# Kernel tuning notes

Hardware: AMD Instinct MI355X
Metric: run time of the kernel (lower is better)

## Reference

```python
import jax, jax.numpy as jnp
import numpy as np

B, T, C, H = 2, 2048, 1024, 16  # head_dim for V = C//H = 64; QK head dim = 3


def setup_inputs() -> dict:
    key = jax.random.key(0)
    ks = jax.random.split(key, 6)
    x = jax.random.normal(ks[0], (B, T, C), dtype=jnp.float32)
    wq = jax.random.normal(ks[1], (C, H * 3), dtype=jnp.float32) * (C ** -0.5)
    wk = jax.random.normal(ks[2], (C, H * 3), dtype=jnp.float32) * (C ** -0.5)
    wv = jax.random.normal(ks[3], (C, C), dtype=jnp.float32) * (C ** -0.5)
    wo = jax.random.normal(ks[4], (C, C), dtype=jnp.float32) * (C ** -0.5)
    dirs = jax.random.normal(ks[5], (H, 3), dtype=jnp.float32)
    head_dirs = dirs / jnp.linalg.norm(dirs, axis=1, keepdims=True)  # unit trigram dirs
    scale = jnp.full((1,), 1.0 / np.sqrt(3.0), dtype=jnp.float32)
    return {"x": x, "wq": wq, "wk": wk, "wv": wv, "wo": wo,
            "head_dirs": head_dirs, "scale": scale}


def reference(x, wq, wk, wv, wo, head_dirs, scale):
    b, t, c = x.shape
    h = head_dirs.shape[0]
    hd = c // h
    # projections: QK live in a 3-dim geometric space per head
    q3 = (x @ wq).reshape(b, t, h, 3).transpose(0, 2, 1, 3)   # (B,H,T,3)
    k3 = (x @ wk).reshape(b, t, h, 3).transpose(0, 2, 1, 3)   # (B,H,T,3)
    v = (x @ wv).reshape(b, t, h, hd).transpose(0, 2, 1, 3)   # (B,H,T,hd)
    # projections of q,k onto per-head trigram directions
    q_on_dir = jnp.einsum('bhtd,hd->bht', q3, head_dirs)      # (B,H,T)
    k_on_dir = jnp.einsum('bhtd,hd->bht', k3, head_dirs)      # (B,H,T)
    dot_scores = jnp.einsum('bhtd,bhsd->bhts', q3, k3) * scale  # (B,H,T,T)
    geo_bias = q_on_dir[..., :, None] * k_on_dir[..., None, :]  # outer product bias
    scores = dot_scores + geo_bias
    causal = jnp.tril(jnp.ones((t, t), dtype=bool))
    scores = jnp.where(causal, scores, -jnp.inf)
    attn = jax.nn.softmax(scores, axis=-1)  # dropout p=0 -> identity
    out = jnp.einsum('bhts,bhsd->bhtd', attn, v)
    out = out.transpose(0, 2, 1, 3).reshape(b, t, c)
    return out @ wo
```

## Files before the change

kernel.cpp:

```cpp
#include <hip/hip_runtime.h>
#include <hip/hip_bf16.h>


typedef short bf16x8 __attribute__((ext_vector_type(8)));
typedef float f32x4 __attribute__((ext_vector_type(4)));
typedef __hip_bfloat16 bf16_t;
typedef unsigned int __attribute__((address_space(1))) u32_as1;
typedef unsigned int __attribute__((address_space(3))) u32_as3;

#define T_SEQ 2048
#define NHEAD 16
#define CDIM 1024
#define L2E 1.4426950408889634f

__device__ __forceinline__ void gl_lds16(const void* g, void* l) {
  __builtin_amdgcn_global_load_lds((const u32_as1*)g, (u32_as3*)l, 16, 0, 0);
}

__device__ __forceinline__ f32x4 mfma16(bf16x8 a, bf16x8 b, f32x4 c) {
  return __builtin_amdgcn_mfma_f32_16x16x32_bf16(a, b, c, 0, 0, 0);
}

__device__ __forceinline__ unsigned short f2bf(float f) {
  __hip_bfloat16 h = __float2bfloat16(f);
  return *(unsigned short*)&h;
}

__device__ __forceinline__ float fast_exp2(float x) {
#if __has_builtin(__builtin_amdgcn_exp2f)
  return __builtin_amdgcn_exp2f(x);
#else
  return exp2f(x);
#endif
}

__global__ __launch_bounds__(256) void k_prep(const float* __restrict__ x,
                                              const float* __restrict__ wq,
                                              const float* __restrict__ wk,
                                              const float* __restrict__ wv,
                                              const float* __restrict__ wo,
                                              bf16_t* __restrict__ xb,
                                              bf16_t* __restrict__ wqkT,
                                              bf16_t* __restrict__ wvT,
                                              bf16_t* __restrict__ woT) {
  __shared__ bf16_t tile[32][33];
  int bid = blockIdx.x, tid = threadIdx.x;
  if (bid < 4096) {
    int i = bid * 256 + tid;
    float4 v = ((const float4*)x)[i];
    ushort4 o;
    o.x = f2bf(v.x); o.y = f2bf(v.y); o.z = f2bf(v.z); o.w = f2bf(v.w);
    ((ushort4*)xb)[i] = o;
    return;
  }
  const float* src; bf16_t* dst; int R, C, bx, by;
  if (bid < 5120)      { int t = bid - 4096; src = wv; dst = wvT;            R = 1024; C = 1024; bx = t & 31; by = t >> 5; }
  else if (bid < 6144) { int t = bid - 5120; src = wo; dst = woT;            R = 1024; C = 1024; bx = t & 31; by = t >> 5; }
  else if (bid < 6208) { int t = bid - 6144; src = wq; dst = wqkT;           R = 1024; C = 48;   bx = t & 1;  by = t >> 1; }
  else                 { int t = bid - 6208; src = wk; dst = wqkT + 48*1024; R = 1024; C = 48;   bx = t & 1;  by = t >> 1; }
  int tx = tid & 31, ty = tid >> 5;
  int r0 = by * 32, c0 = bx * 32;
#pragma unroll
  for (int j = 0; j < 32; j += 8) {
    int r = r0 + ty + j, c = c0 + tx;
    if (r < R && c < C) tile[ty + j][tx] = __float2bfloat16(src[(size_t)r * C + c]);
  }
  __syncthreads();
#pragma unroll
  for (int j = 0; j < 32; j += 8) {
    int c = c0 + ty + j, r = r0 + tx;
    if (r < R && c < C) dst[(size_t)c * R + r] = tile[tx][ty + j];
  }
}

__global__ __launch_bounds__(256) void k_qkproj(const bf16_t* __restrict__ xb,
                                                const bf16_t* __restrict__ wqkT,
                                                const float* __restrict__ head_dirs,
                                                const float* __restrict__ scale,
                                                float* __restrict__ Qt,
                                                float* __restrict__ Kt) {
  __shared__ float red[4][16][96];
  int tid = threadIdx.x, wave = tid >> 6, lane = tid & 63;
  int g = lane >> 4, li = lane & 15;
  int m0 = blockIdx.x * 16;
  f32x4 acc[6] = {};
  int kb = wave * 256;
  for (int k0 = kb; k0 < kb + 256; k0 += 32) {
    bf16x8 a = *(const bf16x8*)(xb + (size_t)(m0 + li) * 1024 + k0 + g * 8);
#pragma unroll
    for (int nt = 0; nt < 6; ++nt) {
      bf16x8 bb = *(const bf16x8*)(wqkT + (size_t)(nt * 16 + li) * 1024 + k0 + g * 8);
      acc[nt] = mfma16(a, bb, acc[nt]);
    }
  }
#pragma unroll
  for (int nt = 0; nt < 6; ++nt)
#pragma unroll
    for (int r = 0; r < 4; ++r) red[wave][g * 4 + r][nt * 16 + li] = acc[nt][r];
  __syncthreads();
  for (int i = tid; i < 16 * 96; i += 256) {
    int row = i / 96, col = i - (i / 96) * 96;
    float v = red[0][row][col] + red[1][row][col] + red[2][row][col] + red[3][row][col];
    if (col >= 48) {
      int n = col - 48;
      int h = n / 3, c = n - h * 3;
      int mg = m0 + row;
      int bb = mg >> 11, tt = mg & 2047;
      Kt[(((size_t)bb * NHEAD + h) * 3 + c) * T_SEQ + tt] = v;
    } else {
      red[0][row][col] = v;
    }
  }
  __syncthreads();
  int row = tid >> 4, h = tid & 15;
  float q0 = red[0][row][h * 3 + 0];
  float q1 = red[0][row][h * 3 + 1];
  float q2 = red[0][row][h * 3 + 2];
  float d0 = head_dirs[h * 3 + 0];
  float d1 = head_dirs[h * 3 + 1];
  float d2 = head_dirs[h * 3 + 2];
  float sc = scale[0] * L2E;
  float dot = (q0 * d0 + q1 * d1 + q2 * d2) * L2E;
  int mg = m0 + row;
  int bb = mg >> 11, tt = mg & 2047;
  size_t base = ((size_t)bb * NHEAD + h) * 3 * T_SEQ + tt;
  Qt[base] = sc * q0 + d0 * dot;
  Qt[base + T_SEQ] = sc * q1 + d1 * dot;
  Qt[base + 2 * T_SEQ] = sc * q2 + d2 * dot;
}

__global__ __launch_bounds__(256) void k_gemm_bt(const bf16_t* __restrict__ A,
                                                 const bf16_t* __restrict__ Bt,
                                                 void* __restrict__ Cout,
                                                 int M, int N, int K, int mode) {
  __shared__ alignas(16) bf16_t As[2][64 * 32];
  __shared__ alignas(16) bf16_t Bs[2][128 * 32];
  int tid = threadIdx.x, wave = tid >> 6, lane = tid & 63;
  int g = lane >> 4, li = lane & 15;
  int n0 = blockIdx.x * 128, m0 = blockIdx.y * 64;
  int wm = wave >> 1, wn = wave & 1;

  const bf16_t* gA0 = A + (size_t)(m0 + (tid >> 2)) * K + (tid & 3) * 8;
  const bf16_t* gB0 = Bt + (size_t)(n0 + (tid >> 2)) * K + (tid & 3) * 8;
  const bf16_t* gB1 = Bt + (size_t)(n0 + 64 + (tid >> 2)) * K + (tid & 3) * 8;

#define GSTAGE(bufi, kk)                                                        \
  {                                                                             \
    gl_lds16(gA0 + (kk), (char*)&As[bufi][0] + (size_t)(wave * 64) * 16);       \
    gl_lds16(gB0 + (kk), (char*)&Bs[bufi][0] + (size_t)(wave * 64) * 16);       \
    gl_lds16(gB1 + (kk), (char*)&Bs[bufi][0] + (size_t)(256 + wave * 64) * 16); \
  }

  f32x4 acc[2][4] = {};
  GSTAGE(0, 0);

  for (int k0 = 0; k0 < K; k0 += 32) {
    int cur = (k0 >> 5) & 1;
    __syncthreads();
    if (k0 + 32 < K) GSTAGE(cur ^ 1, k0 + 32);
    bf16x8 af[2], bfr[4];
#pragma unroll
    for (int mt = 0; mt < 2; ++mt)
      af[mt] = *(const bf16x8*)&As[cur][(wm * 32 + mt * 16 + li) * 32 + g * 8];
#pragma unroll
    for (int nt = 0; nt < 4; ++nt)
      bfr[nt] = *(const bf16x8*)&Bs[cur][(wn * 64 + nt * 16 + li) * 32 + g * 8];
#pragma unroll
    for (int mt = 0; mt < 2; ++mt)
#pragma unroll
      for (int nt = 0; nt < 4; ++nt)
        acc[mt][nt] = mfma16(af[mt], bfr[nt], acc[mt][nt]);
  }
#undef GSTAGE

#pragma unroll
  for (int mt = 0; mt < 2; ++mt)
#pragma unroll
    for (int nt = 0; nt < 4; ++nt)
#pragma unroll
      for (int r = 0; r < 4; ++r) {
        int m = m0 + wm * 32 + mt * 16 + g * 4 + r;
        int n = n0 + wn * 64 + nt * 16 + li;
        float v = acc[mt][nt][r];
        if (mode == 0) {
          int bb = n >> 11, tt = n & 2047;
          ((bf16_t*)Cout)[((size_t)bb * 1024 + m) * T_SEQ + tt] = __float2bfloat16(v);
        } else {
          ((float*)Cout)[(size_t)m * N + n] = v;
        }
      }
}

__global__ __launch_bounds__(256, 4) void k_attn(const float* __restrict__ Qt,
                                                 const float* __restrict__ Kt,
                                                 const bf16_t* __restrict__ VT,
                                                 bf16_t* __restrict__ att) {
  __shared__ alignas(16) bf16_t Vb[2][2][64 * 64];
  __shared__ alignas(16) float Ks[2][3 * 128];
  int tid = threadIdx.x, wave = tid >> 6, lane = tid & 63;
  int g = lane >> 4, li = lane & 15;
  int bid = blockIdx.x;
  int qt = 31 - (bid >> 5);
  int bh = bid & 31;
  int b = bh >> 4, h = bh & 15;
  int mw = wave * 16;

  const float* Qp = Qt + (size_t)bh * 3 * T_SEQ;
  const float* Kp = Kt + (size_t)bh * 3 * T_SEQ;
  const bf16_t* Vp = VT + (size_t)bh * 64 * T_SEQ;

  int tq = qt * 64 + mw + li;
  float q0 = Qp[tq], q1 = Qp[T_SEQ + tq], q2 = Qp[2 * T_SEQ + tq];

  bf16x8 bones;
  unsigned short ob = (li == 0) ? (unsigned short)0x3F80 : (unsigned short)0;
#pragma unroll
  for (int j = 0; j < 8; ++j) bones[j] = (short)ob;

  const bf16_t* vg[2];
#pragma unroll
  for (int p = 0; p < 2; ++p) {
    int P = p * 256 + wave * 64 + lane;
    int d = P >> 3, c = (P & 7) ^ (d & 7);
    vg[p] = Vp + (size_t)d * T_SEQ + c * 8;
  }
  int kch = (wave == 3) ? lane : 32 + lane;
  const float* kg = Kp + (size_t)(kch >> 5) * T_SEQ + (kch & 31) * 4;
  int kbase = (wave == 3) ? 0 : 512;

#define STAGE(bufi, s0v)                                                      \
  {                                                                           \
    _Pragma("unroll") for (int sub_ = 0; sub_ < 2; ++sub_)                    \
        _Pragma("unroll") for (int p_ = 0; p_ < 2; ++p_)                      \
            gl_lds16(vg[p_] + (s0v) + sub_ * 64,                              \
                     (char*)&Vb[bufi][sub_][0] + (p_ * 256 + wave * 64) * 16);\
    if (wave >= 2) gl_lds16(kg + (s0v), (char*)&Ks[bufi][0] + kbase);         \
  }

#define BUILD_AFRAG(MASKED)                                                   \
  _Pragma("unroll") for (int half = 0; half < 2; ++half) {                    \
    int kb = sub * 64 + half * 32 + g * 8;                                    \
    f32x4 kv[3][2];                                                           \
    _Pragma("unroll") for (int c = 0; c < 3; ++c) {                           \
      kv[c][0] = *(const f32x4*)(ks + c * 128 + kb);                          \
      kv[c][1] = *(const f32x4*)(ks + c * 128 + kb + 4);                      \
    }                                                                         \
    _Pragma("unroll") for (int j = 0; j < 8; ++j) {                           \
      float scv = q0 * kv[0][j >> 2][j & 3] + q1 * kv[1][j >> 2][j & 3] +     \
                  q2 * kv[2][j >> 2][j & 3];                                  \
      float pv = fast_exp2(fminf(scv, 115.4f));                               \
      if (MASKED && (bkg + half * 32 + g * 8 + j > tq)) pv = 0.0f;            \
      afrag[half][j] = (short)f2bf(pv);                                       \
    }                                                                         \
  }

  int NT = (qt + 2) >> 1;
  STAGE(0, 0);

  f32x4 acc[5] = {};
  int sw = li & 7;
  int qmin = qt * 64 + mw;
  int qmax = qmin + 15;

  for (int st = 0; st < NT; ++st) {
    int buf = st & 1;
    __syncthreads();
    if (st + 1 < NT) STAGE(buf ^ 1, (st + 1) * 128);
    const float* ks = &Ks[buf][0];
#pragma unroll
    for (int sub = 0; sub < 2; ++sub) {
      int bkg = st * 128 + sub * 64;
      if (bkg > qmax) continue;
      bf16x8 afrag[2];
      if (bkg + 63 > qmin) { BUILD_AFRAG(1) } else { BUILD_AFRAG(0) }
      const bf16_t* vb = &Vb[buf][sub][0];
#pragma unroll
      for (int nt = 0; nt < 4; ++nt) {
        int row = nt * 16 + li;
        bf16x8 b0 = *(const bf16x8*)&vb[row * 64 + (g ^ sw) * 8];
        bf16x8 b1 = *(const bf16x8*)&vb[row * 64 + ((4 + g) ^ sw) * 8];
        acc[nt] = mfma16(afrag[0], b0, acc[nt]);
        acc[nt] = mfma16(afrag[1], b1, acc[nt]);
      }
      acc[4] = mfma16(afrag[0], bones, acc[4]);
      acc[4] = mfma16(afrag[1], bones, acc[4]);
    }
  }
#undef STAGE
#undef BUILD_AFRAG

  float linv[4];
#pragma unroll
  for (int r = 0; r < 4; ++r)
    linv[r] = 1.0f / fmaxf(__shfl(acc[4][r], lane & 48), 1e-35f);

#pragma unroll
  for (int nt = 0; nt < 4; ++nt)
#pragma unroll
    for (int r = 0; r < 4; ++r) {
      int t = qt * 64 + mw + g * 4 + r;
      att[((size_t)b * T_SEQ + t) * CDIM + h * 64 + nt * 16 + li] =
          __float2bfloat16(acc[nt][r] * linv[r]);
    }
}

extern "C" void kernel_launch(void* const* d_in, const int* in_sizes, int n_in,
                              void* d_out, int out_size, void* d_ws, size_t ws_size,
                              hipStream_t stream) {
  const float* x  = (const float*)d_in[0];
  const float* wq = (const float*)d_in[1];
  const float* wk = (const float*)d_in[2];
  const float* wv = (const float*)d_in[3];
  const float* wo = (const float*)d_in[4];
  const float* hd = (const float*)d_in[5];
  const float* sc = (const float*)d_in[6];
  float* out = (float*)d_out;

  char* ws = (char*)d_ws;
  bf16_t* wqkT = (bf16_t*)(ws + 0);
  bf16_t* wvT  = (bf16_t*)(ws + 196608);
  bf16_t* woT  = (bf16_t*)(ws + 2293760);
  float*  Qt   = (float*)(ws + 4390912);
  float*  Kt   = (float*)(ws + 5177344);
  bf16_t* VT   = (bf16_t*)(ws + 5963776);
  bf16_t* att  = (bf16_t*)(ws + 14352384);
  bf16_t* xb   = (bf16_t*)(ws + 22740992);

  k_prep<<<6272, 256, 0, stream>>>(x, wq, wk, wv, wo, xb, wqkT, wvT, woT);

  k_qkproj<<<256, 256, 0, stream>>>(xb, wqkT, hd, sc, Qt, Kt);

  k_gemm_bt<<<dim3(32, 16), 256, 0, stream>>>(wvT, xb, VT, 1024, 4096, 1024, 0);

  k_attn<<<1024, 256, 0, stream>>>(Qt, Kt, VT, att);

  k_gemm_bt<<<dim3(8, 64), 256, 0, stream>>>(att, woT, out, 4096, 1024, 1024, 1);
}
```

Measured before the change: 161.2 us.

## Double GEMM K-step to 64 and interleave causal attention tile order

The GEMM kernel now stages 64 K-elements per iteration instead of 32, so there are half as many barriers and more MFMAs per sync, at the cost of twice the shared memory per block. The attention kernel changes its block-to-query-tile mapping from strictly longest-first to an interleaved pattern that pairs short and long causal tiles. The goal is to balance work across CUs as blocks are dispatched, but it gives up the plain longest-first ordering, which may hurt tail balance.

```diff
diff --git a/kernel.cpp b/kernel.cpp
--- a/kernel.cpp
+++ b/kernel.cpp
@@ -133,8 +133,8 @@
                                                  const bf16_t* __restrict__ Bt,
                                                  void* __restrict__ Cout,
                                                  int M, int N, int K, int mode) {
-  __shared__ alignas(16) bf16_t As[2][64 * 32];
-  __shared__ alignas(16) bf16_t Bs[2][128 * 32];
+  __shared__ alignas(16) bf16_t As[2][2 * 64 * 32];
+  __shared__ alignas(16) bf16_t Bs[2][2 * 128 * 32];
   int tid = threadIdx.x, wave = tid >> 6, lane = tid & 63;
   int g = lane >> 4, li = lane & 15;
   int n0 = blockIdx.x * 128, m0 = blockIdx.y * 64;
@@ -144,32 +144,40 @@
   const bf16_t* gB0 = Bt + (size_t)(n0 + (tid >> 2)) * K + (tid & 3) * 8;
   const bf16_t* gB1 = Bt + (size_t)(n0 + 64 + (tid >> 2)) * K + (tid & 3) * 8;
 
-#define GSTAGE(bufi, kk)                                                        \
-  {                                                                             \
-    gl_lds16(gA0 + (kk), (char*)&As[bufi][0] + (size_t)(wave * 64) * 16);       \
-    gl_lds16(gB0 + (kk), (char*)&Bs[bufi][0] + (size_t)(wave * 64) * 16);       \
-    gl_lds16(gB1 + (kk), (char*)&Bs[bufi][0] + (size_t)(256 + wave * 64) * 16); \
+#define GSTAGE(bufi, kk)                                          \
+  {                                                               \
+    char* aB = (char*)&As[bufi][0];                               \
+    char* bB = (char*)&Bs[bufi][0];                               \
+    gl_lds16(gA0 + (kk), aB + tid * 16);                          \
+    gl_lds16(gA0 + (kk) + 32, aB + (256 + tid) * 16);             \
+    gl_lds16(gB0 + (kk), bB + tid * 16);                          \
+    gl_lds16(gB1 + (kk), bB + (256 + tid) * 16);                  \
+    gl_lds16(gB0 + (kk) + 32, bB + (512 + tid) * 16);             \
+    gl_lds16(gB1 + (kk) + 32, bB + (768 + tid) * 16);             \
   }
 
   f32x4 acc[2][4] = {};
   GSTAGE(0, 0);
 
-  for (int k0 = 0; k0 < K; k0 += 32) {
-    int cur = (k0 >> 5) & 1;
+  for (int k0 = 0; k0 < K; k0 += 64) {
+    int cur = (k0 >> 6) & 1;
     __syncthreads();
-    if (k0 + 32 < K) GSTAGE(cur ^ 1, k0 + 32);
-    bf16x8 af[2], bfr[4];
-#pragma unroll
-    for (int mt = 0; mt < 2; ++mt)
-      af[mt] = *(const bf16x8*)&As[cur][(wm * 32 + mt * 16 + li) * 32 + g * 8];
-#pragma unroll
-    for (int nt = 0; nt < 4; ++nt)
-      bfr[nt] = *(const bf16x8*)&Bs[cur][(wn * 64 + nt * 16 + li) * 32 + g * 8];
-#pragma unroll
-    for (int mt = 0; mt < 2; ++mt)
+    if (k0 + 64 < K) GSTAGE(cur ^ 1, k0 + 64);
+#pragma unroll
+    for (int kk = 0; kk < 2; ++kk) {
+      bf16x8 af[2], bfr[4];
+#pragma unroll
+      for (int mt = 0; mt < 2; ++mt)
+        af[mt] = *(const bf16x8*)&As[cur][kk * 2048 + (wm * 32 + mt * 16 + li) * 32 + g * 8];
 #pragma unroll
       for (int nt = 0; nt < 4; ++nt)
-        acc[mt][nt] = mfma16(af[mt], bfr[nt], acc[mt][nt]);
+        bfr[nt] = *(const bf16x8*)&Bs[cur][kk * 4096 + (wn * 64 + nt * 16 + li) * 32 + g * 8];
+#pragma unroll
+      for (int mt = 0; mt < 2; ++mt)
+#pragma unroll
+        for (int nt = 0; nt < 4; ++nt)
+          acc[mt][nt] = mfma16(af[mt], bfr[nt], acc[mt][nt]);
+    }
   }
 #undef GSTAGE
 
@@ -200,8 +208,9 @@
   int tid = threadIdx.x, wave = tid >> 6, lane = tid & 63;
   int g = lane >> 4, li = lane & 15;
   int bid = blockIdx.x;
-  int qt = 31 - (bid >> 5);
-  int bh = bid & 31;
+  int p = bid >> 5, bh = bid & 31;
+  int a = p & 7, bq = p >> 3;
+  int qt = (bq == 0) ? a : (bq == 1) ? 31 - a : (bq == 2) ? 8 + a : 23 - a;
   int b = bh >> 4, h = bh & 15;
   int mw = wave * 16;
 
@@ -219,10 +228,10 @@
 
   const bf16_t* vg[2];
 #pragma unroll
-  for (int p = 0; p < 2; ++p) {
-    int P = p * 256 + wave * 64 + lane;
+  for (int pp = 0; pp < 2; ++pp) {
+    int P = pp * 256 + wave * 64 + lane;
     int d = P >> 3, c = (P & 7) ^ (d & 7);
-    vg[p] = Vp + (size_t)d * T_SEQ + c * 8;
+    vg[pp] = Vp + (size_t)d * T_SEQ + c * 8;
   }
   int kch = (wave == 3) ? lane : 32 + lane;
   const float* kg = Kp + (size_t)(kch >> 5) * T_SEQ + (kch & 31) * 4;
```

Result: faster. 157.8 us (-2.1%).
